# Kernel tuning notes

Measured on AMD Instinct MI355X. Metric: run time of the kernel, lower is better.

Reference implementation:

```python
import jax, jax.numpy as jnp
import numpy as np

B, T, D, P, C = 65536, 3, 512, 32, 10  # batch, views, x_dim, p_dim, num_classes

def setup_inputs() -> dict:
    key = jax.random.key(0)
    ks = jax.random.split(key, 6)
    return {
        "x": jax.random.normal(ks[0], (B, T, D), dtype=jnp.float32),
        "Wk": jax.random.normal(ks[1], (P, D), dtype=jnp.float32) * (1.0 / np.sqrt(D)),
        "Wv": jax.random.normal(ks[2], (P, D), dtype=jnp.float32) * (1.0 / np.sqrt(D)),
        "Wq": jax.random.normal(ks[3], (P, T * D), dtype=jnp.float32) * (1.0 / np.sqrt(T * D)),
        "Wfc": jax.random.normal(ks[4], (C, P), dtype=jnp.float32) * (1.0 / np.sqrt(P)),
        "bfc": jax.random.normal(ks[5], (C,), dtype=jnp.float32) * 0.01,
    }

def reference(x, Wk, Wv, Wq, Wfc, bfc):
    # x: [B, 3, D]. Per-sample: k_i = Wk x_i, v_i = Wv x_i, q = Wq concat(x1,x2,x3)
    k = jnp.einsum('btd,pd->btp', x, Wk)                 # [B,3,P]
    v = jnp.einsum('btd,pd->btp', x, Wv)                 # [B,3,P]
    q = jnp.einsum('bf,pf->bp', x.reshape(x.shape[0], -1), Wq)  # [B,P]
    a = jax.nn.softmax(jnp.einsum('bp,btp->bt', q, k), axis=-1)  # 3-way softmax [B,3]
    c = jnp.einsum('bt,btp->bp', a, v)                   # weighted sum [B,P]
    return c @ Wfc.T + bfc                               # [B,C]
```

## Files before the change

kernel.cpp:

```cpp
#include <hip/hip_runtime.h>


typedef __attribute__((ext_vector_type(4))) float  f32x4;
typedef __attribute__((ext_vector_type(8))) _Float16 h16x8;

#define T_VIEWS 3
#define D_DIM   512
#define P_DIM   32
#define C_DIM   10
#define NROWS   80
#define NT      5
#define KC      16
#define M_TILES 2
#define M_WAVE  (M_TILES*16)
#define WAVES_PER_BLOCK 4
#define SAMPLES_PER_BLOCK (M_WAVE*WAVES_PER_BLOCK)

__global__ void build_weights(const float* __restrict__ Wk,
                              const float* __restrict__ Wv,
                              const float* __restrict__ Wq,
                              const float* __restrict__ Wfc,
                              _Float16* __restrict__ Wf) {
    const int row = blockIdx.x;
    const int t   = row / NROWS;
    const int j   = row % NROWS;
    const int d   = threadIdx.x;
    float val;
    if (j < 32) {
        val = Wk[j * D_DIM + d];
    } else if (j < 64) {
        const int p = j - 32;
        val = Wq[p * (T_VIEWS * D_DIM) + t * D_DIM + d];
    } else if (j < 64 + C_DIM) {
        const int i = j - 64;
        float s = 0.f;
        #pragma unroll
        for (int p = 0; p < P_DIM; ++p)
            s += Wfc[i * P_DIM + p] * Wv[p * D_DIM + d];
        val = s;
    } else {
        val = 0.f;
    }
    const int n = j >> 4, col = j & 15;
    const int kc = d >> 5, r = d & 31, quad = r >> 3, jj = r & 7;
    const size_t addr = (size_t)((((t * KC + kc) * NT + n) * 64) + quad * 16 + col) * 8 + jj;
    Wf[addr] = (_Float16)val;
}

__global__ __launch_bounds__(256) void attn_fused(
        const float* __restrict__ x,
        const _Float16* __restrict__ Wf,
        const float* __restrict__ bfc,
        float* __restrict__ out) {
    const int lane = threadIdx.x & 63;
    const int wave = threadIdx.x >> 6;
    const int col  = lane & 15;
    const int quad = lane >> 4;
    const int row_base = blockIdx.x * SAMPLES_PER_BLOCK + wave * M_WAVE;

    f32x4 acc[3][M_TILES][NT];
    #pragma unroll
    for (int t = 0; t < 3; ++t)
        #pragma unroll
        for (int m = 0; m < M_TILES; ++m)
            #pragma unroll
            for (int n = 0; n < NT; ++n)
                acc[t][m][n] = (f32x4)0.f;

    const float* xbase = x + (size_t)(row_base + col) * (T_VIEWS * D_DIM) + quad * 8;

    #pragma unroll
    for (int t = 0; t < 3; ++t) {
        const _Float16* wt = Wf + (size_t)t * (KC * NT * 512) + lane * 8;
        #pragma unroll 2
        for (int kc = 0; kc < KC; ++kc) {
            h16x8 b[NT];
            #pragma unroll
            for (int n = 0; n < NT; ++n)
                b[n] = *(const h16x8*)(wt + (kc * NT + n) * 512);
            #pragma unroll
            for (int m = 0; m < M_TILES; ++m) {
                const float* xp = xbase + t * D_DIM + (size_t)m * 16 * (T_VIEWS * D_DIM) + kc * 32;
                const f32x4 x0 = __builtin_nontemporal_load((const f32x4*)xp);
                const f32x4 x1 = __builtin_nontemporal_load((const f32x4*)(xp + 4));
                h16x8 a;
                #pragma unroll
                for (int i = 0; i < 4; ++i) {
                    a[i]     = (_Float16)x0[i];
                    a[i + 4] = (_Float16)x1[i];
                }
                #pragma unroll
                for (int n = 0; n < NT; ++n)
                    acc[t][m][n] = __builtin_amdgcn_mfma_f32_16x16x32_f16(a, b[n], acc[t][m][n], 0, 0, 0);
            }
        }
    }

    const float bias = (col < C_DIM) ? bfc[col] : 0.f;

    #pragma unroll
    for (int m = 0; m < M_TILES; ++m) {
        float outv[4];
        #pragma unroll
        for (int r = 0; r < 4; ++r) {
            const float qa = acc[0][m][2][r] + acc[1][m][2][r] + acc[2][m][2][r];
            const float qb = acc[0][m][3][r] + acc[1][m][3][r] + acc[2][m][3][r];
            float s0 = qa * acc[0][m][0][r] + qb * acc[0][m][1][r];
            float s1 = qa * acc[1][m][0][r] + qb * acc[1][m][1][r];
            float s2 = qa * acc[2][m][0][r] + qb * acc[2][m][1][r];
            #pragma unroll
            for (int msk = 1; msk <= 8; msk <<= 1) {
                s0 += __shfl_xor(s0, msk, 64);
                s1 += __shfl_xor(s1, msk, 64);
                s2 += __shfl_xor(s2, msk, 64);
            }
            const float mx = fmaxf(s0, fmaxf(s1, s2));
            const float e0 = __expf(s0 - mx);
            const float e1 = __expf(s1 - mx);
            const float e2 = __expf(s2 - mx);
            const float inv = 1.f / (e0 + e1 + e2);
            outv[r] = (e0 * acc[0][m][4][r] + e1 * acc[1][m][4][r] + e2 * acc[2][m][4][r]) * inv + bias;
        }
        if (col < C_DIM) {
            const int b0 = row_base + m * 16 + quad * 4;
            #pragma unroll
            for (int r = 0; r < 4; ++r)
                out[(size_t)(b0 + r) * C_DIM + col] = outv[r];
        }
    }
}

extern "C" void kernel_launch(void* const* d_in, const int* in_sizes, int n_in,
                              void* d_out, int out_size, void* d_ws, size_t ws_size,
                              hipStream_t stream) {
    const float* x   = (const float*)d_in[0];
    const float* Wk  = (const float*)d_in[1];
    const float* Wv  = (const float*)d_in[2];
    const float* Wq  = (const float*)d_in[3];
    const float* Wfc = (const float*)d_in[4];
    const float* bfc = (const float*)d_in[5];
    _Float16* Wf = (_Float16*)d_ws;

    hipLaunchKernelGGL(build_weights, dim3(T_VIEWS * NROWS), dim3(D_DIM), 0, stream,
                       Wk, Wv, Wq, Wfc, Wf);

    const int B_TOTAL = in_sizes[0] / (T_VIEWS * D_DIM);
    const int blocks = B_TOTAL / SAMPLES_PER_BLOCK;
    hipLaunchKernelGGL(attn_fused, dim3(blocks), dim3(256), 0, stream,
                       x, Wf, bfc, (float*)d_out);
}
```

Baseline: 540.3 us.

## Shrink per-wave tile to 16 samples and share q accumulators across views

Each wave now handles one 16-sample M tile instead of two, and the q accumulators are summed across views inside the MFMA chain rather than held per view, which cuts accumulator registers from 30 to 10 vectors. Launch bounds now request 4 blocks per CU to raise occupancy and hide latency on the memory-bound x stream. The K-dimension permutation changes so each lane loads two 16-byte chunks 64 bytes apart instead of 32 contiguous bytes, and the weight layout is permuted to match. The cost is twice as many blocks and half the reuse of each weight fragment load per MFMA.

```diff
diff --git a/kernel.cpp b/kernel.cpp
--- a/kernel.cpp
+++ b/kernel.cpp
@@ -11,10 +11,8 @@
 #define NROWS   80
 #define NT      5
 #define KC      16
-#define M_TILES 2
-#define M_WAVE  (M_TILES*16)
 #define WAVES_PER_BLOCK 4
-#define SAMPLES_PER_BLOCK (M_WAVE*WAVES_PER_BLOCK)
+#define SAMPLES_PER_BLOCK (16 * WAVES_PER_BLOCK)
 
 __global__ void build_weights(const float* __restrict__ Wk,
                               const float* __restrict__ Wv,
@@ -41,13 +39,15 @@
     } else {
         val = 0.f;
     }
-    const int n = j >> 4, col = j & 15;
-    const int kc = d >> 5, r = d & 31, quad = r >> 3, jj = r & 7;
-    const size_t addr = (size_t)((((t * KC + kc) * NT + n) * 64) + quad * 16 + col) * 8 + jj;
+    const int n = j >> 4, coln = j & 15;
+    const int kc = d >> 5, r = d & 31;
+    const int quad = (r >> 2) & 3;
+    const int jj   = ((r >> 4) << 2) | (r & 3);
+    const size_t addr = (size_t)((((t * KC + kc) * NT + n) * 64) + quad * 16 + coln) * 8 + jj;
     Wf[addr] = (_Float16)val;
 }
 
-__global__ __launch_bounds__(256) void attn_fused(
+__global__ __launch_bounds__(256, 4) void attn_fused(
         const float* __restrict__ x,
         const _Float16* __restrict__ Wf,
         const float* __restrict__ bfc,
@@ -56,77 +56,76 @@
     const int wave = threadIdx.x >> 6;
     const int col  = lane & 15;
     const int quad = lane >> 4;
-    const int row_base = blockIdx.x * SAMPLES_PER_BLOCK + wave * M_WAVE;
+    const int row_base = blockIdx.x * SAMPLES_PER_BLOCK + wave * 16;
 
-    f32x4 acc[3][M_TILES][NT];
+    f32x4 acc_k[3][2];
+    f32x4 acc_q[2];
+    f32x4 acc_y[3];
     #pragma unroll
-    for (int t = 0; t < 3; ++t)
-        #pragma unroll
-        for (int m = 0; m < M_TILES; ++m)
-            #pragma unroll
-            for (int n = 0; n < NT; ++n)
-                acc[t][m][n] = (f32x4)0.f;
+    for (int t = 0; t < 3; ++t) {
+        acc_k[t][0] = (f32x4)0.f;
+        acc_k[t][1] = (f32x4)0.f;
+        acc_y[t]    = (f32x4)0.f;
+    }
+    acc_q[0] = (f32x4)0.f;
+    acc_q[1] = (f32x4)0.f;
 
-    const float* xbase = x + (size_t)(row_base + col) * (T_VIEWS * D_DIM) + quad * 8;
+    const float* xbase = x + (size_t)(row_base + col) * (T_VIEWS * D_DIM) + quad * 4;
+    const _Float16* wt = Wf + lane * 8;
 
     #pragma unroll
     for (int t = 0; t < 3; ++t) {
-        const _Float16* wt = Wf + (size_t)t * (KC * NT * 512) + lane * 8;
         #pragma unroll 2
         for (int kc = 0; kc < KC; ++kc) {
             h16x8 b[NT];
             #pragma unroll
             for (int n = 0; n < NT; ++n)
-                b[n] = *(const h16x8*)(wt + (kc * NT + n) * 512);
+                b[n] = *(const h16x8*)(wt + (size_t)(((t * KC + kc) * NT + n)) * 512);
+            const float* xp = xbase + t * D_DIM + kc * 32;
+            const f32x4 x0 = __builtin_nontemporal_load((const f32x4*)xp);
+            const f32x4 x1 = __builtin_nontemporal_load((const f32x4*)(xp + 16));
+            h16x8 a;
             #pragma unroll
-            for (int m = 0; m < M_TILES; ++m) {
-                const float* xp = xbase + t * D_DIM + (size_t)m * 16 * (T_VIEWS * D_DIM) + kc * 32;
-                const f32x4 x0 = __builtin_nontemporal_load((const f32x4*)xp);
-                const f32x4 x1 = __builtin_nontemporal_load((const f32x4*)(xp + 4));
-                h16x8 a;
-                #pragma unroll
-                for (int i = 0; i < 4; ++i) {
-                    a[i]     = (_Float16)x0[i];
-                    a[i + 4] = (_Float16)x1[i];
-                }
-                #pragma unroll
-                for (int n = 0; n < NT; ++n)
-                    acc[t][m][n] = __builtin_amdgcn_mfma_f32_16x16x32_f16(a, b[n], acc[t][m][n], 0, 0, 0);
+            for (int i = 0; i < 4; ++i) {
+                a[i]     = (_Float16)x0[i];
+                a[i + 4] = (_Float16)x1[i];
             }
+            acc_k[t][0] = __builtin_amdgcn_mfma_f32_16x16x32_f16(a, b[0], acc_k[t][0], 0, 0, 0);
+            acc_k[t][1] = __builtin_amdgcn_mfma_f32_16x16x32_f16(a, b[1], acc_k[t][1], 0, 0, 0);
+            acc_q[0]    = __builtin_amdgcn_mfma_f32_16x16x32_f16(a, b[2], acc_q[0],    0, 0, 0);
+            acc_q[1]    = __builtin_amdgcn_mfma_f32_16x16x32_f16(a, b[3], acc_q[1],    0, 0, 0);
+            acc_y[t]    = __builtin_amdgcn_mfma_f32_16x16x32_f16(a, b[4], acc_y[t],    0, 0, 0);
         }
     }
 
     const float bias = (col < C_DIM) ? bfc[col] : 0.f;
 
+    float outv[4];
     #pragma unroll
-    for (int m = 0; m < M_TILES; ++m) {
-        float outv[4];
+    for (int r = 0; r < 4; ++r) {
+        const float qa = acc_q[0][r];
+        const float qb = acc_q[1][r];
+        float s0 = qa * acc_k[0][0][r] + qb * acc_k[0][1][r];
+        float s1 = qa * acc_k[1][0][r] + qb * acc_k[1][1][r];
+        float s2 = qa * acc_k[2][0][r] + qb * acc_k[2][1][r];
         #pragma unroll
-        for (int r = 0; r < 4; ++r) {
-            const float qa = acc[0][m][2][r] + acc[1][m][2][r] + acc[2][m][2][r];
-            const float qb = acc[0][m][3][r] + acc[1][m][3][r] + acc[2][m][3][r];
-            float s0 = qa * acc[0][m][0][r] + qb * acc[0][m][1][r];
-            float s1 = qa * acc[1][m][0][r] + qb * acc[1][m][1][r];
-            float s2 = qa * acc[2][m][0][r] + qb * acc[2][m][1][r];
-            #pragma unroll
-            for (int msk = 1; msk <= 8; msk <<= 1) {
-                s0 += __shfl_xor(s0, msk, 64);
-                s1 += __shfl_xor(s1, msk, 64);
-                s2 += __shfl_xor(s2, msk, 64);
-            }
-            const float mx = fmaxf(s0, fmaxf(s1, s2));
-            const float e0 = __expf(s0 - mx);
-            const float e1 = __expf(s1 - mx);
-            const float e2 = __expf(s2 - mx);
-            const float inv = 1.f / (e0 + e1 + e2);
-            outv[r] = (e0 * acc[0][m][4][r] + e1 * acc[1][m][4][r] + e2 * acc[2][m][4][r]) * inv + bias;
+        for (int msk = 1; msk <= 8; msk <<= 1) {
+            s0 += __shfl_xor(s0, msk, 64);
+            s1 += __shfl_xor(s1, msk, 64);
+            s2 += __shfl_xor(s2, msk, 64);
         }
-        if (col < C_DIM) {
-            const int b0 = row_base + m * 16 + quad * 4;
-            #pragma unroll
-            for (int r = 0; r < 4; ++r)
-                out[(size_t)(b0 + r) * C_DIM + col] = outv[r];
-        }
+        const float mx = fmaxf(s0, fmaxf(s1, s2));
+        const float e0 = __expf(s0 - mx);
+        const float e1 = __expf(s1 - mx);
+        const float e2 = __expf(s2 - mx);
+        const float inv = 1.f / (e0 + e1 + e2);
+        outv[r] = (e0 * acc_y[0][r] + e1 * acc_y[1][r] + e2 * acc_y[2][r]) * inv + bias;
+    }
+    if (col < C_DIM) {
+        const int b0 = row_base + quad * 4;
+        #pragma unroll
+        for (int r = 0; r < 4; ++r)
+            out[(size_t)(b0 + r) * C_DIM + col] = outv[r];
     }
 }
 
```

Result: slower. 561.5 us (+3.9%).
